# Performance work log

Hardware: AMD Instinct MI355X
Metric: run time of the kernel (lower is better)

The kernel has to match this reference:

```python
import jax, jax.numpy as jnp
import numpy as np

N_SEG = 128      # number of ragged segments (len(leng))
TOTAL = 32768    # total rows = sum(leng)
D = 1280         # cnn_feature (tf_efficientnet_b0 classifier.in_features)
D_HEAD = 512     # hidden of logits head


def setup_inputs() -> dict:
    key = jax.random.key(0)
    ks = jax.random.split(key, 8)
    # ragged lengths (static at trace time), summing exactly to TOTAL
    rng = np.random.default_rng(0)
    leng = rng.integers(64, 448, size=N_SEG).astype(np.int64)
    leng = np.maximum((leng * (TOTAL / leng.sum())).astype(np.int64), 1)
    leng[-1] += TOTAL - leng.sum()
    segment_ids = jnp.asarray(np.repeat(np.arange(N_SEG), leng), jnp.int32)

    features = jax.random.normal(ks[0], (TOTAL, D), jnp.float32)
    s = 0.02
    Ww = jax.random.normal(ks[1], (D, D), jnp.float32) * s        # proj_w.weight
    bw = jnp.zeros((D,), jnp.float32)                              # proj_w.bias
    v = jax.random.normal(ks[2], (D,), jnp.float32) * s           # proj_v.weight (1,D) squeezed
    W1 = jax.random.normal(ks[3], (D_HEAD, D), jnp.float32) * s   # logits[0].weight
    b1 = jnp.zeros((D_HEAD,), jnp.float32)
    W2 = jax.random.normal(ks[4], (1, D_HEAD), jnp.float32) * s   # logits[3].weight
    b2 = jnp.zeros((1,), jnp.float32)
    return {"features": features, "Ww": Ww, "bw": bw, "v": v,
            "W1": W1, "b1": b1, "W2": W2, "b2": b2,
            "segment_ids": segment_ids}


def reference(features, Ww, bw, v, W1, b1, W2, b2, segment_ids):
    # per-row attention logits: tanh(x @ Ww^T + bw) @ v    -> [TOTAL]
    H = jnp.tanh(features @ Ww.T + bw)
    s = H @ v
    # segment-wise stable softmax (replaces Python loop over leng)
    m = jax.ops.segment_max(s, segment_ids, num_segments=N_SEG)
    e = jnp.exp(s - m[segment_ids])
    z = jax.ops.segment_sum(e, segment_ids, num_segments=N_SEG)
    att = e / z[segment_ids]                                      # [TOTAL]
    # attention-weighted sum pooling per segment -> [N_SEG, D]
    pooled = jax.ops.segment_sum(features * att[:, None], segment_ids,
                                 num_segments=N_SEG)
    # logits head (dropout is identity in eval)
    h = jax.nn.relu(pooled @ W1.T + b1)
    return h @ W2.T + b2                                          # [N_SEG, 1]
```

## Files before the change

### kernel.cpp

```cpp
#include <hip/hip_runtime.h>
#include <hip/hip_bf16.h>


#define TOTAL_ROWS 32768
#define DIM 1280
#define NSEG 128
#define DHEAD 512
#define NKT 20
#define NPART 4

typedef _Float16 f16x8 __attribute__((ext_vector_type(8)));
typedef _Float16 f16x4 __attribute__((ext_vector_type(4)));
typedef float f32x4 __attribute__((ext_vector_type(4)));

#define OFF_XH   0
#define OFF_WH   83886080
#define OFF_S    87162880
#define OFF_SEG  87425024
#define OFF_POOL 87426048
#define OFF_H    88081408
#define OFF_PP   OFF_WH

__device__ __forceinline__ void load_lds16(const void* g, void* l) {
  __builtin_amdgcn_global_load_lds(
      (const __attribute__((address_space(1))) unsigned int*)g,
      (__attribute__((address_space(3))) unsigned int*)l, 16, 0, 0);
}

__device__ __forceinline__ float tanh_fast(float x) {
  float e = __expf(2.0f * x);
  return 1.0f - 2.0f * __builtin_amdgcn_rcpf(e + 1.0f);
}

__global__ void cvt_init_kernel(const float* __restrict__ a, _Float16* __restrict__ oa,
                                int na8, const float* __restrict__ b,
                                _Float16* __restrict__ ob, int nb8,
                                const int* __restrict__ sid,
                                int* __restrict__ segstart, float* __restrict__ s) {
  int i = blockIdx.x * blockDim.x + threadIdx.x;
  if (i < TOTAL_ROWS) {
    s[i] = 0.f;
    int sg = sid[i];
    if (i == 0) segstart[0] = 0;
    else if (sid[i - 1] != sg) segstart[sg] = i;
    if (i == TOTAL_ROWS - 1) segstart[sg + 1] = TOTAL_ROWS;
  }
  const float* in;
  _Float16* out;
  int idx;
  if (i < na8) {
    in = a; out = oa; idx = i;
  } else {
    idx = i - na8;
    if (idx >= nb8) return;
    in = b; out = ob;
  }
  const float4* p = (const float4*)in + (size_t)idx * 2;
  float4 u0 = p[0], u1 = p[1];
  f16x8 h;
  h[0] = (_Float16)u0.x; h[1] = (_Float16)u0.y;
  h[2] = (_Float16)u0.z; h[3] = (_Float16)u0.w;
  h[4] = (_Float16)u1.x; h[5] = (_Float16)u1.y;
  h[6] = (_Float16)u1.z; h[7] = (_Float16)u1.w;
  *((f16x8*)out + idx) = h;
}

__global__ __launch_bounds__(512, 2) void gemm_s_kernel(
    const _Float16* __restrict__ X, const _Float16* __restrict__ W,
    const float* __restrict__ v, const float* __restrict__ bw,
    float* __restrict__ s) {
  __shared__ _Float16 As[2][2][8192];
  __shared__ _Float16 Bs[2][2][8192];

  const int rowBase = blockIdx.x * 256;
  const int jBase = blockIdx.y * 256;
  const int t = threadIdx.x;
  const int lane = t & 63;
  const int w = t >> 6;
  const int wm = w >> 2;
  const int wn = w & 3;
  const int lm = lane & 15;
  const int kc = lane >> 4;
  const int bh = wn >> 1;

  const int subrow = lane >> 3;
  const int g = ((lane & 7) - subrow) & 7;
  const _Float16* gA = X + (size_t)(rowBase + w * 8 + subrow) * DIM + g * 8;
  const _Float16* gB = W + (size_t)(jBase + w * 8 + subrow) * DIM + g * 8;

  int aOff[2], bOff[2];
#pragma unroll
  for (int ks = 0; ks < 2; ++ks) {
    int swz = ((ks * 4 + kc + lm) & 7) * 8;
    aOff[ks] = lm * 64 + swz;
    bOff[ks] = ((wn & 1) * 64 + lm) * 64 + swz;
  }

  f32x4 acc[8][4];
  const f32x4 zero = {0.f, 0.f, 0.f, 0.f};
#pragma unroll
  for (int i = 0; i < 8; ++i)
#pragma unroll
    for (int j = 0; j < 4; ++j) acc[i][j] = zero;

  f16x8 a[4][2], b[4][2];

#define STAGE_A(BUF, HALF, TT) do { \
    const _Float16* _src = gA + (size_t)(HALF) * 128 * DIM + (size_t)(TT) * 64; \
    load_lds16(_src, &As[BUF][HALF][w * 512]); \
    load_lds16(_src + 64 * DIM, &As[BUF][HALF][4096 + w * 512]); \
  } while (0)
#define STAGE_B(BUF, HALF, TT) do { \
    const _Float16* _src = gB + (size_t)(HALF) * 128 * DIM + (size_t)(TT) * 64; \
    load_lds16(_src, &Bs[BUF][HALF][w * 512]); \
    load_lds16(_src + 64 * DIM, &Bs[BUF][HALF][4096 + w * 512]); \
  } while (0)

#define READ_A1(BUF, SLOT, MT) do { \
    _Pragma("unroll") for (int ks = 0; ks < 2; ++ks) \
      a[SLOT][ks] = *(const f16x8*)&As[BUF][wm][aOff[ks] + (MT) * 1024]; \
  } while (0)
#define READ_B(BUF) do { \
    _Pragma("unroll") for (int nt = 0; nt < 4; ++nt) \
    _Pragma("unroll") for (int ks = 0; ks < 2; ++ks) \
      b[nt][ks] = *(const f16x8*)&Bs[BUF][bh][bOff[ks] + nt * 1024]; \
  } while (0)
#define MFMA_ROW(SLOT, ROW) do { \
    _Pragma("unroll") for (int nt = 0; nt < 4; ++nt) \
    _Pragma("unroll") for (int ks = 0; ks < 2; ++ks) \
      acc[ROW][nt] = __builtin_amdgcn_mfma_f32_16x16x32_f16( \
          a[SLOT][ks], b[nt][ks], acc[ROW][nt], 0, 0, 0); \
  } while (0)

#define CFENCE asm volatile("" ::: "memory")
#define WAIT_VM4 asm volatile("s_waitcnt vmcnt(4)" ::: "memory")
#define WAIT_VM0 asm volatile("s_waitcnt vmcnt(0)" ::: "memory")
#define BAR __builtin_amdgcn_s_barrier()
#define SCHED0 __builtin_amdgcn_sched_barrier(0)
#define SETP1 __builtin_amdgcn_s_setprio(1)
#define SETP0 __builtin_amdgcn_s_setprio(0)

#define KTILE(BUF, SA, SB, TAILWAIT) do { \
    CFENCE; \
     \
    READ_B(BUF); \
    READ_A1(BUF, 0, 0); READ_A1(BUF, 1, 1); \
    SA; \
    SETP1; \
    MFMA_ROW(0, 0); \
    READ_A1(BUF, 2, 2); \
    MFMA_ROW(1, 1); \
    READ_A1(BUF, 3, 3); \
    MFMA_ROW(2, 2); \
    MFMA_ROW(3, 3); \
    SETP0; \
    SCHED0; BAR; CFENCE; \
     \
    READ_A1(BUF, 0, 4); READ_A1(BUF, 1, 5); \
    SB; \
    SETP1; \
    MFMA_ROW(0, 4); \
    READ_A1(BUF, 2, 6); \
    MFMA_ROW(1, 5); \
    READ_A1(BUF, 3, 7); \
    MFMA_ROW(2, 6); \
    MFMA_ROW(3, 7); \
    SETP0; \
    TAILWAIT; SCHED0; BAR; \
  } while (0)

  STAGE_A(0, 0, 0); STAGE_A(0, 1, 0);
  STAGE_B(0, 0, 0); STAGE_B(0, 1, 0);
  STAGE_B(1, 0, 1); STAGE_B(1, 1, 1);
  WAIT_VM4;
  BAR;

  for (int kt = 0; kt < NKT - 2; kt += 2) {
    KTILE(0,
          { STAGE_A(1, 0, kt + 1); STAGE_A(1, 1, kt + 1); },
          { STAGE_B(0, 0, kt + 2); STAGE_B(0, 1, kt + 2); },
          WAIT_VM4);
    KTILE(1,
          { STAGE_A(0, 0, kt + 2); STAGE_A(0, 1, kt + 2); },
          { STAGE_B(1, 0, kt + 3); STAGE_B(1, 1, kt + 3); },
          WAIT_VM4);
  }
  KTILE(0,
        { STAGE_A(1, 0, NKT - 1); STAGE_A(1, 1, NKT - 1); },
        (void)0, WAIT_VM0);
  KTILE(1, (void)0, (void)0, (void)0);

#undef KTILE
#undef STAGE_A
#undef STAGE_B
#undef READ_A1
#undef READ_B
#undef MFMA_ROW

  const int colBase = jBase + wn * 64 + lm;
  float vv[4], bb[4];
#pragma unroll
  for (int nt = 0; nt < 4; ++nt) {
    int j = colBase + nt * 16;
    vv[nt] = v[j];
    bb[nt] = bw[j];
  }
  const int gq = lane >> 4;
#pragma unroll
  for (int mt = 0; mt < 8; ++mt) {
#pragma unroll
    for (int r = 0; r < 4; ++r) {
      float sumv = 0.f;
#pragma unroll
      for (int nt = 0; nt < 4; ++nt)
        sumv += tanh_fast(acc[mt][nt][r] + bb[nt]) * vv[nt];
      sumv += __shfl_xor(sumv, 1);
      sumv += __shfl_xor(sumv, 2);
      sumv += __shfl_xor(sumv, 4);
      sumv += __shfl_xor(sumv, 8);
      if (lm == 0) {
        int row = rowBase + wm * 128 + mt * 16 + gq * 4 + r;
        atomicAdd(&s[row], sumv);
      }
    }
  }
}

__global__ void softpool_kernel(const _Float16* __restrict__ F,
                                const float* __restrict__ s,
                                const int* __restrict__ segstart,
                                float* __restrict__ pooledp) {
  int seg = blockIdx.x, part = blockIdx.y;
  int st = segstart[seg], en = segstart[seg + 1];
  int t = threadIdx.x;
  __shared__ float redm[5], redz[5];
  float m = -1e30f;
  for (int i = st + t; i < en; i += 320) m = fmaxf(m, s[i]);
  for (int d = 1; d < 64; d <<= 1) m = fmaxf(m, __shfl_xor(m, d));
  if ((t & 63) == 0) redm[t >> 6] = m;
  __syncthreads();
  m = fmaxf(fmaxf(fmaxf(redm[0], redm[1]), fmaxf(redm[2], redm[3])), redm[4]);
  float z = 0.f;
  for (int i = st + t; i < en; i += 320) z += __expf(s[i] - m);
  for (int d = 1; d < 64; d <<= 1) z += __shfl_xor(z, d);
  if ((t & 63) == 0) redz[t >> 6] = z;
  __syncthreads();
  z = redz[0] + redz[1] + redz[2] + redz[3] + redz[4];
  float rz = 1.0f / z;

  int len = en - st;
  int chunk = (len + NPART - 1) / NPART;
  int r0 = st + chunk * part;
  int r1 = min(en, r0 + chunk);
  float acc[4] = {0.f, 0.f, 0.f, 0.f};
  int r = r0;
  for (; r + 2 <= r1; r += 2) {
    float a0 = __expf(s[r] - m) * rz;
    float a1 = __expf(s[r + 1] - m) * rz;
    f16x4 f0 = ((const f16x4*)(F + (size_t)r * DIM))[t];
    f16x4 f1 = ((const f16x4*)(F + (size_t)(r + 1) * DIM))[t];
#pragma unroll
    for (int c = 0; c < 4; ++c) {
      acc[c] = fmaf(a0, (float)f0[c], acc[c]);
      acc[c] = fmaf(a1, (float)f1[c], acc[c]);
    }
  }
  if (r < r1) {
    float a0 = __expf(s[r] - m) * rz;
    f16x4 f0 = ((const f16x4*)(F + (size_t)r * DIM))[t];
#pragma unroll
    for (int c = 0; c < 4; ++c) acc[c] = fmaf(a0, (float)f0[c], acc[c]);
  }
  float4 o;
  o.x = acc[0]; o.y = acc[1]; o.z = acc[2]; o.w = acc[3];
  *(float4*)(pooledp + ((size_t)part * NSEG + seg) * DIM + t * 4) = o;
}

__global__ void fold_kernel(const float* __restrict__ pp,
                            float* __restrict__ pooled) {
  int i = blockIdx.x * 256 + threadIdx.x;
  pooled[i] = pp[i] + pp[i + NSEG * DIM] + pp[i + 2 * NSEG * DIM] +
              pp[i + 3 * NSEG * DIM];
}

__global__ void head1_kernel(const float* __restrict__ pooled,
                             const float* __restrict__ W1,
                             const float* __restrict__ b1, float* __restrict__ h) {
  int og = blockIdx.x, sg = blockIdx.y;
  __shared__ float Wt[16 * 65];
  __shared__ float Pt[32 * 65];
  int t = threadIdx.x;
  int tx = t & 15, ty = t >> 4;
  float acc0 = 0.f, acc1 = 0.f;
  for (int kcc = 0; kcc < 20; ++kcc) {
    __syncthreads();
#pragma unroll
    for (int u = 0; u < 4; ++u) {
      int lin = t + 256 * u;
      int o = lin >> 6, kk = lin & 63;
      Wt[o * 65 + kk] = W1[(size_t)(og * 16 + o) * DIM + kcc * 64 + kk];
    }
#pragma unroll
    for (int u = 0; u < 8; ++u) {
      int lin = t + 256 * u;
      int ss = lin >> 6, kk = lin & 63;
      Pt[ss * 65 + kk] = pooled[(size_t)(sg * 32 + ss) * DIM + kcc * 64 + kk];
    }
    __syncthreads();
#pragma unroll
    for (int kk = 0; kk < 64; ++kk) {
      float wv = Wt[tx * 65 + kk];
      acc0 = fmaf(Pt[ty * 65 + kk], wv, acc0);
      acc1 = fmaf(Pt[(ty + 16) * 65 + kk], wv, acc1);
    }
  }
  int o = og * 16 + tx;
  float bias = b1[o];
  h[(size_t)(sg * 32 + ty) * DHEAD + o] = fmaxf(acc0 + bias, 0.f);
  h[(size_t)(sg * 32 + ty + 16) * DHEAD + o] = fmaxf(acc1 + bias, 0.f);
}

__global__ void head2_kernel(const float* __restrict__ h,
                             const float* __restrict__ W2,
                             const float* __restrict__ b2, float* __restrict__ out) {
  int seg = blockIdx.x;
  int t = threadIdx.x;
  float val = h[(size_t)seg * DHEAD + t] * W2[t] +
              h[(size_t)seg * DHEAD + t + 256] * W2[t + 256];
  for (int d = 1; d < 64; d <<= 1) val += __shfl_xor(val, d);
  __shared__ float red[4];
  if ((t & 63) == 0) red[t >> 6] = val;
  __syncthreads();
  if (t == 0) out[seg] = red[0] + red[1] + red[2] + red[3] + b2[0];
}

extern "C" void kernel_launch(void* const* d_in, const int* in_sizes, int n_in,
                              void* d_out, int out_size, void* d_ws, size_t ws_size,
                              hipStream_t stream) {
  const float* features = (const float*)d_in[0];
  const float* Ww = (const float*)d_in[1];
  const float* bw = (const float*)d_in[2];
  const float* v = (const float*)d_in[3];
  const float* W1 = (const float*)d_in[4];
  const float* b1 = (const float*)d_in[5];
  const float* W2 = (const float*)d_in[6];
  const float* b2 = (const float*)d_in[7];
  const int* segids = (const int*)d_in[8];
  float* out = (float*)d_out;

  char* ws = (char*)d_ws;
  _Float16* Xh = (_Float16*)(ws + OFF_XH);
  _Float16* Wh = (_Float16*)(ws + OFF_WH);
  float* s = (float*)(ws + OFF_S);
  int* segstart = (int*)(ws + OFF_SEG);
  float* pooled = (float*)(ws + OFF_POOL);
  float* pooledp = (float*)(ws + OFF_PP);
  float* h = (float*)(ws + OFF_H);

  const int na8 = TOTAL_ROWS * DIM / 8;
  const int nb8 = DIM * DIM / 8;
  cvt_init_kernel<<<(na8 + nb8 + 255) / 256, 256, 0, stream>>>(
      features, Xh, na8, Ww, Wh, nb8, segids, segstart, s);

  dim3 ggrid(TOTAL_ROWS / 256, DIM / 256);
  gemm_s_kernel<<<ggrid, 512, 0, stream>>>(Xh, Wh, v, bw, s);

  softpool_kernel<<<dim3(NSEG, NPART), 320, 0, stream>>>(Xh, s, segstart, pooledp);
  fold_kernel<<<NSEG * DIM / 256, 256, 0, stream>>>(pooledp, pooled);
  head1_kernel<<<dim3(32, 4), 256, 0, stream>>>(pooled, W1, b1, h);
  head2_kernel<<<NSEG, 256, 0, stream>>>(h, W2, b2, out);
}
```

Baseline: 453.3 us.

## Triple-buffer A tiles in LDS to deepen prefetch in the scoring GEMM

The A operand in shared memory goes from two buffers to three, with a six-k-tile unrolled loop that rotates A buffers mod 3 and B buffers mod 2. A loads are now issued two k-tiles ahead, at the start of each k-tile and before the LDS reads. The wait threshold rises from 4 to 8 outstanding loads, so more global-to-LDS traffic stays in flight while MFMAs run. This raises the block's LDS footprint to about 160 KB, which leaves no room for anything else and rules out a second block per CU.

```diff
diff --git a/kernel.cpp b/kernel.cpp
--- a/kernel.cpp
+++ b/kernel.cpp
@@ -69,7 +69,7 @@
     const _Float16* __restrict__ X, const _Float16* __restrict__ W,
     const float* __restrict__ v, const float* __restrict__ bw,
     float* __restrict__ s) {
-  __shared__ _Float16 As[2][2][8192];
+  __shared__ _Float16 As[3][2][8192];
   __shared__ _Float16 Bs[2][2][8192];
 
   const int rowBase = blockIdx.x * 256;
@@ -115,15 +115,17 @@
     load_lds16(_src, &Bs[BUF][HALF][w * 512]); \
     load_lds16(_src + 64 * DIM, &Bs[BUF][HALF][4096 + w * 512]); \
   } while (0)
-
-#define READ_A1(BUF, SLOT, MT) do { \
+#define SA2(DBUF, TT) do { STAGE_A(DBUF, 0, TT); STAGE_A(DBUF, 1, TT); } while (0)
+#define SB2(DBUF, TT) do { STAGE_B(DBUF, 0, TT); STAGE_B(DBUF, 1, TT); } while (0)
+
+#define READ_A1(BA, SLOT, MT) do { \
     _Pragma("unroll") for (int ks = 0; ks < 2; ++ks) \
-      a[SLOT][ks] = *(const f16x8*)&As[BUF][wm][aOff[ks] + (MT) * 1024]; \
-  } while (0)
-#define READ_B(BUF) do { \
+      a[SLOT][ks] = *(const f16x8*)&As[BA][wm][aOff[ks] + (MT) * 1024]; \
+  } while (0)
+#define READ_B(BB) do { \
     _Pragma("unroll") for (int nt = 0; nt < 4; ++nt) \
     _Pragma("unroll") for (int ks = 0; ks < 2; ++ks) \
-      b[nt][ks] = *(const f16x8*)&Bs[BUF][bh][bOff[ks] + nt * 1024]; \
+      b[nt][ks] = *(const f16x8*)&Bs[BB][bh][bOff[ks] + nt * 1024]; \
   } while (0)
 #define MFMA_ROW(SLOT, ROW) do { \
     _Pragma("unroll") for (int nt = 0; nt < 4; ++nt) \
@@ -133,66 +135,63 @@
   } while (0)
 
 #define CFENCE asm volatile("" ::: "memory")
-#define WAIT_VM4 asm volatile("s_waitcnt vmcnt(4)" ::: "memory")
+#define WAIT_VM8 asm volatile("s_waitcnt vmcnt(8)" ::: "memory")
 #define WAIT_VM0 asm volatile("s_waitcnt vmcnt(0)" ::: "memory")
 #define BAR __builtin_amdgcn_s_barrier()
 #define SCHED0 __builtin_amdgcn_sched_barrier(0)
 #define SETP1 __builtin_amdgcn_s_setprio(1)
 #define SETP0 __builtin_amdgcn_s_setprio(0)
 
-#define KTILE(BUF, SA, SB, TAILWAIT) do { \
+#define KTILE(BA, BB, SA, SB, TAILWAIT) do { \
     CFENCE; \
      \
-    READ_B(BUF); \
-    READ_A1(BUF, 0, 0); READ_A1(BUF, 1, 1); \
     SA; \
+    READ_B(BB); \
+    READ_A1(BA, 0, 0); READ_A1(BA, 1, 1); \
     SETP1; \
     MFMA_ROW(0, 0); \
-    READ_A1(BUF, 2, 2); \
+    READ_A1(BA, 2, 2); \
     MFMA_ROW(1, 1); \
-    READ_A1(BUF, 3, 3); \
+    READ_A1(BA, 3, 3); \
     MFMA_ROW(2, 2); \
     MFMA_ROW(3, 3); \
     SETP0; \
     SCHED0; BAR; CFENCE; \
      \
-    READ_A1(BUF, 0, 4); READ_A1(BUF, 1, 5); \
     SB; \
+    READ_A1(BA, 0, 4); READ_A1(BA, 1, 5); \
     SETP1; \
     MFMA_ROW(0, 4); \
-    READ_A1(BUF, 2, 6); \
+    READ_A1(BA, 2, 6); \
     MFMA_ROW(1, 5); \
-    READ_A1(BUF, 3, 7); \
+    READ_A1(BA, 3, 7); \
     MFMA_ROW(2, 6); \
     MFMA_ROW(3, 7); \
     SETP0; \
     TAILWAIT; SCHED0; BAR; \
   } while (0)
 
-  STAGE_A(0, 0, 0); STAGE_A(0, 1, 0);
-  STAGE_B(0, 0, 0); STAGE_B(0, 1, 0);
-  STAGE_B(1, 0, 1); STAGE_B(1, 1, 1);
-  WAIT_VM4;
+  SA2(0, 0); SB2(0, 0);
+  SA2(1, 1); SB2(1, 1);
+  WAIT_VM8;
   BAR;
 
-  for (int kt = 0; kt < NKT - 2; kt += 2) {
-    KTILE(0,
-          { STAGE_A(1, 0, kt + 1); STAGE_A(1, 1, kt + 1); },
-          { STAGE_B(0, 0, kt + 2); STAGE_B(0, 1, kt + 2); },
-          WAIT_VM4);
-    KTILE(1,
-          { STAGE_A(0, 0, kt + 2); STAGE_A(0, 1, kt + 2); },
-          { STAGE_B(1, 0, kt + 3); STAGE_B(1, 1, kt + 3); },
-          WAIT_VM4);
-  }
-  KTILE(0,
-        { STAGE_A(1, 0, NKT - 1); STAGE_A(1, 1, NKT - 1); },
-        (void)0, WAIT_VM0);
-  KTILE(1, (void)0, (void)0, (void)0);
+  for (int kt = 0; kt < NKT - 2; kt += 6) {
+    KTILE(0, 0, SA2(2, kt + 2), SB2(0, kt + 2), WAIT_VM8);
+    KTILE(1, 1, SA2(0, kt + 3), SB2(1, kt + 3), WAIT_VM8);
+    KTILE(2, 0, SA2(1, kt + 4), SB2(0, kt + 4), WAIT_VM8);
+    KTILE(0, 1, SA2(2, kt + 5), SB2(1, kt + 5), WAIT_VM8);
+    KTILE(1, 0, SA2(0, kt + 6), SB2(0, kt + 6), WAIT_VM8);
+    KTILE(2, 1, SA2(1, kt + 7), SB2(1, kt + 7), WAIT_VM8);
+  }
+  KTILE(0, 0, (void)0, (void)0, WAIT_VM0);
+  KTILE(1, 1, (void)0, (void)0, (void)0);
 
 #undef KTILE
 #undef STAGE_A
 #undef STAGE_B
+#undef SA2
+#undef SB2
 #undef READ_A1
 #undef READ_B
 #undef MFMA_ROW
```

Result: no change. 451.2 us (-0.5%).
